# Performance work log

Hardware: AMD Instinct MI355X
Metric: run time of the kernel (lower is better)

The kernel has to match this reference:

```python
import jax, jax.numpy as jnp
import numpy as np

B, N, D = 16, 16384, 256
H, W = 128, 128  # N == H*W: coords cover the grid exactly once (collision-free scatter)
K = 3


def setup_inputs() -> dict:
    key = jax.random.key(0)
    k1, k2, k3, k4 = jax.random.split(key, 4)
    x = jax.random.normal(k1, (B, N, D), dtype=jnp.float32)
    # coords: per-batch random permutation of all grid cells -> unique (gx, gy) per batch
    perm = jax.vmap(lambda k: jax.random.permutation(k, H * W))(jax.random.split(k2, B))  # (B, N)
    gx = perm % W
    gy = perm // W
    coords = jnp.stack([gx, gy], axis=-1).astype(jnp.int32)  # (B, N, 2), [...,0]=x, [...,1]=y
    # depthwise Conv2d params: weight (D, 1, K, K), bias (D,)  (torch kaiming-uniform-ish scale)
    bound = 1.0 / np.sqrt(K * K)
    conv_w = jax.random.uniform(k3, (D, 1, K, K), minval=-bound, maxval=bound, dtype=jnp.float32)
    conv_b = jax.random.uniform(k4, (D,), minval=-bound, maxval=bound, dtype=jnp.float32)
    return {"x": x, "coords": coords, "conv_w": conv_w, "conv_b": conv_b}


def reference(x, coords, conv_w, conv_b):
    b, n, d = x.shape
    # normalize coords to zero-based bounding box (per batch min, as in torch)
    min_c = coords.min(axis=1, keepdims=True)
    gc = coords - min_c
    max_c = gc.max(axis=1).max(axis=0)
    Hh = int(max_c[1]) + 1
    Ww = int(max_c[0]) + 1
    if Hh * Ww > 256 * 256:
        return x  # safety guard: skip mixing
    gx = gc[..., 0]
    gy = gc[..., 1]
    flat = gy * Ww + gx  # (B, N) flattened spatial index
    x_T = jnp.swapaxes(x, 1, 2)  # (B, D, N)
    # scatter: (B, D, H*W) dense grid, one vmap'd scatter per batch element
    scatter = lambda xt, f: jnp.zeros((d, Hh * Ww), x.dtype).at[:, f].set(xt)
    grid = jax.vmap(scatter)(x_T, flat).reshape(b, d, Hh, Ww)
    # depthwise conv (groups = D) with SAME-style padding k//2, then exact (erf) GELU
    out_grid = jax.lax.conv_general_dilated(
        grid, conv_w,
        window_strides=(1, 1),
        padding=[(K // 2, K // 2), (K // 2, K // 2)],
        feature_group_count=d,
    ) + conv_b[None, :, None, None]
    out_grid = jax.nn.gelu(out_grid, approximate=False)
    # gather back at the same positions, residual add
    out_flat = out_grid.reshape(b, d, Hh * Ww)
    gathered = jax.vmap(lambda g, f: g[:, f])(out_flat, flat)  # (B, D, N)
    return x + jnp.swapaxes(gathered, 1, 2)
```

## Files before the change

### kernel.cpp

```cpp
#include <hip/hip_runtime.h>
#include <hip/hip_bf16.h>

#define BB 16
#define NN 16384
#define DD 256
#define GW 128


__global__ __launch_bounds__(256) void build_inv_kernel(
    const int* __restrict__ coords, int* __restrict__ inv) {
  int i = blockIdx.x * blockDim.x + threadIdx.x;
  int b = i >> 14;
  int gx = coords[2 * (size_t)i];
  int gy = coords[2 * (size_t)i + 1];
  inv[(b << 14) + (gy << 7) + gx] = i & (NN - 1);
}

__global__ __launch_bounds__(256) void mixer_kernel(
    const float* __restrict__ x, const float* __restrict__ cw,
    const float* __restrict__ cb, const int* __restrict__ inv,
    float* __restrict__ out) {
  __shared__ int s_inv[36];

  const int id = blockIdx.x;
  const int Br = id & 7;
  const int rem = id >> 3;
  const int p = rem & 63;
  const int Bq = rem >> 6;
  const int band = Bq * 8 + Br;
  const int b = band >> 4;
  const int band_in = band & 15;
  const int prow = p >> 5;
  const int pcol = p & 31;
  const int gy0 = band_in * 8 + prow * 4;
  const int gx0 = pcol * 4;

  const int c = threadIdx.x;

  float w[9];
#pragma unroll
  for (int j = 0; j < 9; ++j) w[j] = cw[c * 9 + j];
  const float bias = cb[c];

  if (c < 36) {
    const int wy = c / 6, wx = c % 6;
    const int gy = gy0 - 1 + wy, gx = gx0 - 1 + wx;
    int nv = -1;
    if ((unsigned)gy < (unsigned)GW && (unsigned)gx < (unsigned)GW)
      nv = inv[(b << 14) + (gy << 7) + gx];
    s_inv[c] = nv;
  }
  __syncthreads();

  const float* __restrict__ xb = x + (((size_t)b << 14) << 8);
  float v[36];
#pragma unroll
  for (int s = 0; s < 36; ++s) {
    const int ns = s_inv[s];
    v[s] = (ns >= 0) ? xb[((size_t)ns << 8) + c] : 0.0f;
  }

  float acc[16];
#pragma unroll
  for (int i = 0; i < 16; ++i) acc[i] = bias;
#pragma unroll
  for (int iy = 0; iy < 4; ++iy)
#pragma unroll
    for (int ix = 0; ix < 4; ++ix)
#pragma unroll
      for (int ky = 0; ky < 3; ++ky)
#pragma unroll
        for (int kx = 0; kx < 3; ++kx)
          acc[iy * 4 + ix] =
              fmaf(w[ky * 3 + kx], v[(iy + ky) * 6 + (ix + kx)],
                   acc[iy * 4 + ix]);

  float* __restrict__ ob = out + (((size_t)b << 14) << 8);
#pragma unroll
  for (int iy = 0; iy < 4; ++iy)
#pragma unroll
    for (int ix = 0; ix < 4; ++ix) {
      const int n = s_inv[(iy + 1) * 6 + (ix + 1)];
      const float a = acc[iy * 4 + ix];
      const float g = 0.5f * a * (1.0f + erff(a * 0.70710678118654752f));
      ob[((size_t)n << 8) + c] = v[(iy + 1) * 6 + (ix + 1)] + g;
    }
}

extern "C" void kernel_launch(void* const* d_in, const int* in_sizes, int n_in,
                              void* d_out, int out_size, void* d_ws,
                              size_t ws_size, hipStream_t stream) {
  const float* x = (const float*)d_in[0];
  const int* coords = (const int*)d_in[1];
  const float* cw = (const float*)d_in[2];
  const float* cb = (const float*)d_in[3];
  float* out = (float*)d_out;
  int* inv = (int*)d_ws;

  {
    dim3 grid((BB * NN) / 256), block(256);
    build_inv_kernel<<<grid, block, 0, stream>>>(coords, inv);
  }
  {
    dim3 grid(BB * NN / 16), block(256);
    mixer_kernel<<<grid, block, 0, stream>>>(x, cw, cb, inv, out);
  }
}
```

Measured before the change: 125.3 us.

## Use 16x16 spatial tiles with rolling 3-row register window in mixer

Each block now processes a 16x16 grid tile (18x18 halo) instead of a 4x4 tile, and streams rows through a 4-row rotating register buffer. This cuts halo re-reads of x from 36/16 loads per output to about 1.27, reducing global traffic. It also makes the gathered indices uniform via readfirstlane and writes outputs with nontemporal stores. The trade-off is far fewer blocks (1024) and higher register pressure, which may hurt occupancy and latency hiding.

```diff
diff --git a/kernel.cpp b/kernel.cpp
--- a/kernel.cpp
+++ b/kernel.cpp
@@ -5,7 +5,8 @@
 #define NN 16384
 #define DD 256
 #define GW 128
-
+#define TS 16
+#define HS 18
 
 __global__ __launch_bounds__(256) void build_inv_kernel(
     const int* __restrict__ coords, int* __restrict__ inv) {
@@ -20,20 +21,14 @@
     const float* __restrict__ x, const float* __restrict__ cw,
     const float* __restrict__ cb, const int* __restrict__ inv,
     float* __restrict__ out) {
-  __shared__ int s_inv[36];
+  __shared__ int s_inv[HS][HS];
 
   const int id = blockIdx.x;
-  const int Br = id & 7;
   const int rem = id >> 3;
-  const int p = rem & 63;
-  const int Bq = rem >> 6;
-  const int band = Bq * 8 + Br;
-  const int b = band >> 4;
-  const int band_in = band & 15;
-  const int prow = p >> 5;
-  const int pcol = p & 31;
-  const int gy0 = band_in * 8 + prow * 4;
-  const int gx0 = pcol * 4;
+  const int b = ((id & 7) << 1) + (rem >> 6);
+  const int tile = rem & 63;
+  const int gy0 = (tile >> 3) * TS;
+  const int gx0 = (tile & 7) * TS;
 
   const int c = threadIdx.x;
 
@@ -42,49 +37,65 @@
   for (int j = 0; j < 9; ++j) w[j] = cw[c * 9 + j];
   const float bias = cb[c];
 
-  if (c < 36) {
-    const int wy = c / 6, wx = c % 6;
+  for (int t = c; t < HS * HS; t += 256) {
+    const int wy = t / HS, wx = t % HS;
     const int gy = gy0 - 1 + wy, gx = gx0 - 1 + wx;
     int nv = -1;
     if ((unsigned)gy < (unsigned)GW && (unsigned)gx < (unsigned)GW)
       nv = inv[(b << 14) + (gy << 7) + gx];
-    s_inv[c] = nv;
+    s_inv[wy][wx] = nv;
   }
   __syncthreads();
 
-  const float* __restrict__ xb = x + (((size_t)b << 14) << 8);
-  float v[36];
+  const float* __restrict__ xb = x + ((size_t)b << 22);
+  float* __restrict__ ob = out + ((size_t)b << 22);
+
+  float v[4][HS];
 #pragma unroll
-  for (int s = 0; s < 36; ++s) {
-    const int ns = s_inv[s];
-    v[s] = (ns >= 0) ? xb[((size_t)ns << 8) + c] : 0.0f;
+  for (int r = 0; r < 3; ++r) {
+#pragma unroll
+    for (int j = 0; j < HS; ++j) {
+      int ns = __builtin_amdgcn_readfirstlane(s_inv[r][j]);
+      v[r][j] = (ns >= 0) ? xb[((size_t)ns << 8) + c] : 0.0f;
+    }
   }
 
-  float acc[16];
+#pragma unroll 4
+  for (int iy = 0; iy < TS; ++iy) {
+    if (iy + 3 < HS) {
 #pragma unroll
-  for (int i = 0; i < 16; ++i) acc[i] = bias;
+      for (int j = 0; j < HS; ++j) {
+        int ns = __builtin_amdgcn_readfirstlane(s_inv[iy + 3][j]);
+        v[(iy + 3) & 3][j] = (ns >= 0) ? xb[((size_t)ns << 8) + c] : 0.0f;
+      }
+    }
+    const float* r0 = v[iy & 3];
+    const float* r1 = v[(iy + 1) & 3];
+    const float* r2 = v[(iy + 2) & 3];
+
+    float acc[TS];
 #pragma unroll
-  for (int iy = 0; iy < 4; ++iy)
+    for (int ix = 0; ix < TS; ++ix) {
+      float a = bias;
+      a = fmaf(w[0], r0[ix], a);
+      a = fmaf(w[1], r0[ix + 1], a);
+      a = fmaf(w[2], r0[ix + 2], a);
+      a = fmaf(w[3], r1[ix], a);
+      a = fmaf(w[4], r1[ix + 1], a);
+      a = fmaf(w[5], r1[ix + 2], a);
+      a = fmaf(w[6], r2[ix], a);
+      a = fmaf(w[7], r2[ix + 1], a);
+      a = fmaf(w[8], r2[ix + 2], a);
+      acc[ix] = a;
+    }
 #pragma unroll
-    for (int ix = 0; ix < 4; ++ix)
-#pragma unroll
-      for (int ky = 0; ky < 3; ++ky)
-#pragma unroll
-        for (int kx = 0; kx < 3; ++kx)
-          acc[iy * 4 + ix] =
-              fmaf(w[ky * 3 + kx], v[(iy + ky) * 6 + (ix + kx)],
-                   acc[iy * 4 + ix]);
-
-  float* __restrict__ ob = out + (((size_t)b << 14) << 8);
-#pragma unroll
-  for (int iy = 0; iy < 4; ++iy)
-#pragma unroll
-    for (int ix = 0; ix < 4; ++ix) {
-      const int n = s_inv[(iy + 1) * 6 + (ix + 1)];
-      const float a = acc[iy * 4 + ix];
+    for (int ix = 0; ix < TS; ++ix) {
+      const int n = __builtin_amdgcn_readfirstlane(s_inv[iy + 1][ix + 1]);
+      const float a = acc[ix];
       const float g = 0.5f * a * (1.0f + erff(a * 0.70710678118654752f));
-      ob[((size_t)n << 8) + c] = v[(iy + 1) * 6 + (ix + 1)] + g;
+      __builtin_nontemporal_store(r1[ix + 1] + g, &ob[((size_t)n << 8) + c]);
     }
+  }
 }
 
 extern "C" void kernel_launch(void* const* d_in, const int* in_sizes, int n_in,
@@ -102,7 +113,7 @@
     build_inv_kernel<<<grid, block, 0, stream>>>(coords, inv);
   }
   {
-    dim3 grid(BB * NN / 16), block(256);
+    dim3 grid(BB * (GW / TS) * (GW / TS)), block(256);
     mixer_kernel<<<grid, block, 0, stream>>>(x, cw, cb, inv, out);
   }
 }
```

Result: faster. 120.3 us (-4.0%).
